# Kernel optimization log

Hardware: AMD Instinct MI355X
Metric: run time of the kernel (lower is better)

Reference implementation:

```python
import jax, jax.numpy as jnp
import numpy as np
import math

CH = 256
NH = 8
HD = CH // NH
GROUPS = 32
EPS = 1e-5


def group_norm(x, gamma, beta):
    # x: [B, C, H, W]; normalize over (C//GROUPS, H, W) per group
    B, C, H, W = x.shape
    xg = x.reshape(B, GROUPS, C // GROUPS, H, W)
    mean = xg.mean(axis=(2, 3, 4), keepdims=True)
    var = xg.var(axis=(2, 3, 4), keepdims=True)
    xg = (xg - mean) * jax.lax.rsqrt(var + EPS)
    x = xg.reshape(B, C, H, W)
    return x * gamma[None, :, None, None] + beta[None, :, None, None]


def setup_inputs() -> dict:
    key = jax.random.key(0)
    ks = jax.random.split(key, 7)
    B, H, W = 2, 64, 64
    x = jax.random.normal(ks[0], (B, CH, H, W), dtype=jnp.float32)
    # conv1x1 weights stored as [out, in] (kernel 1x1 squeezed)
    w_qkv = jax.random.normal(ks[1], (3 * CH, CH), dtype=jnp.float32) * (1.0 / math.sqrt(CH))
    b_qkv = jax.random.normal(ks[2], (3 * CH,), dtype=jnp.float32) * 0.01
    w_proj = jax.random.normal(ks[3], (CH, CH), dtype=jnp.float32) * (1.0 / math.sqrt(CH))
    b_proj = jax.random.normal(ks[4], (CH,), dtype=jnp.float32) * 0.01
    gn_gamma = jnp.ones((CH,), dtype=jnp.float32)
    gn_beta = jnp.zeros((CH,), dtype=jnp.float32)
    return {"x": x, "w_qkv": w_qkv, "b_qkv": b_qkv, "w_proj": w_proj,
            "b_proj": b_proj, "gn_gamma": gn_gamma, "gn_beta": gn_beta}


def reference(x, w_qkv, b_qkv, w_proj, b_proj, gn_gamma, gn_beta):
    B, C, H, W = x.shape
    HW = H * W
    h = group_norm(x, gn_gamma, gn_beta)
    # 1x1 conv == channel matmul
    qkv = jnp.einsum('bchw,oc->bohw', h, w_qkv) + b_qkv[None, :, None, None]
    q, k, v = jnp.split(qkv, 3, axis=1)  # each [B, C, H, W]
    # reshape to heads: q,v -> [B, NH, HW, HD]; k -> [B, NH, HD, HW]
    q = q.reshape(B, NH, HD, HW).transpose(0, 1, 3, 2)
    k = k.reshape(B, NH, HD, HW)
    v = v.reshape(B, NH, HD, HW).transpose(0, 1, 3, 2)
    scale = 1.0 / math.sqrt(HD)
    attn = jnp.einsum('bnqd,bndk->bnqk', q, k) * scale  # [B, NH, HW, HW]
    attn = jax.nn.softmax(attn, axis=-1)
    out = jnp.einsum('bnqk,bnkd->bnqd', attn, v)  # [B, NH, HW, HD]
    out = out.transpose(0, 1, 3, 2).reshape(B, C, H, W)
    out = jnp.einsum('bchw,oc->bohw', out, w_proj) + b_proj[None, :, None, None]
    return x + out
```

## Files before the change

kernel.cpp:

```cpp
#include <hip/hip_runtime.h>
#include <hip/hip_bf16.h>


typedef __attribute__((ext_vector_type(8))) __bf16 bf16x8;
typedef __attribute__((ext_vector_type(4))) float f32x4;
typedef __attribute__((ext_vector_type(2))) float f32x2;
typedef __attribute__((ext_vector_type(16))) float f32x16;
typedef __attribute__((ext_vector_type(2))) unsigned int uint32x2;

#define HW 4096
#define C 256
#define NH 8
#define HD 32
#define QSCALE 0.25505654f
#define KST 36
#define VST 68
#define TST 36
#define NSPLIT 4

__device__ inline unsigned short f2bf(float f) {
  union { float f; unsigned int u; } v; v.f = f;
  unsigned int u = v.u;
  return (unsigned short)((u + 0x7fffu + ((u >> 16) & 1u)) >> 16);
}

__device__ inline bf16x8 load8(const unsigned short* p) {
  bf16x8 v;
  __builtin_memcpy(&v, __builtin_assume_aligned(p, 16), 16);
  return v;
}

__device__ inline bf16x8 load8_lds(const unsigned short* p) {
  uint2 a = *(const uint2*)__builtin_assume_aligned(p, 8);
  uint2 b = *(const uint2*)__builtin_assume_aligned(p + 4, 8);
  union { uint4 u; bf16x8 v; } cv;
  cv.u = make_uint4(a.x, a.y, b.x, b.y);
  return cv.v;
}

__device__ inline unsigned int fbits(float f) {
  unsigned int u; __builtin_memcpy(&u, &f, 4); return u;
}
__device__ inline float bits2f(unsigned int u) {
  float f; __builtin_memcpy(&f, &u, 4); return f;
}

__device__ inline unsigned int pack_bf2(float lo, float hi) {
  return __builtin_amdgcn_perm(fbits(hi) + 0x8000u, fbits(lo) + 0x8000u, 0x07060302u);
}
__device__ inline unsigned int pack_bf2t(float lo, float hi) {
  return __builtin_amdgcn_perm(fbits(hi), fbits(lo), 0x07060302u);
}

__device__ inline size_t toff(int row, int col) {
  return ((size_t)(row >> 6) * 8 + (col >> 5)) * 2048 + (row & 63) * 32 + (col & 31);
}

__global__ __launch_bounds__(256) void gn_stats_part(const float* __restrict__ x,
                                                     float* __restrict__ parts,
                                                     const float* __restrict__ wq,
                                                     const float* __restrict__ wp,
                                                     unsigned short* __restrict__ wq_t,
                                                     unsigned short* __restrict__ wp_t) {
  if (blockIdx.x >= 256) {
    int base = (blockIdx.x - 256) * 1024 + threadIdx.x * 4;
    #pragma unroll
    for (int k = 0; k < 4; k++) {
      int idx = base + k;
      if (idx < 196608) {
        int o = idx >> 8, c = idx & 255;
        wq_t[toff(o, c)] = f2bf(wq[idx]);
      } else {
        int i2 = idx - 196608;
        int o = i2 >> 8, c = i2 & 255;
        wp_t[toff(o, c)] = f2bf(wp[i2]);
      }
    }
    return;
  }
  int i = blockIdx.x;
  const float4* p4 = (const float4*)(x + (size_t)i * 8192);
  int t = threadIdx.x;
  float s = 0.f, ss = 0.f;
  for (int k = t; k < 2048; k += 256) {
    float4 v = p4[k];
    s  += v.x + v.y + v.z + v.w;
    ss += v.x*v.x + v.y*v.y + v.z*v.z + v.w*v.w;
  }
  for (int m = 32; m >= 1; m >>= 1) {
    s  += __shfl_down(s, m, 64);
    ss += __shfl_down(ss, m, 64);
  }
  __shared__ float red[8];
  int w = t >> 6;
  if ((t & 63) == 0) { red[w] = s; red[w + 4] = ss; }
  __syncthreads();
  if (t == 0) {
    parts[i]       = red[0] + red[1] + red[2] + red[3];
    parts[256 + i] = red[4] + red[5] + red[6] + red[7];
  }
}

__global__ __launch_bounds__(256) void gn_apply(const float* __restrict__ x,
                                                const float* __restrict__ parts,
                                                const float* __restrict__ gamma,
                                                const float* __restrict__ beta,
                                                unsigned short* __restrict__ h_t) {
  __shared__ float tile[64][65];
  __shared__ float gmean[8], grstd[8];
  int b = blockIdx.z, c0 = blockIdx.y * 64, s0 = blockIdx.x * 64;
  int t = threadIdx.x;
  if (t < 8) {
    int bg = b * 32 + (c0 >> 3) + t;
    float s  = (parts[4*bg] + parts[4*bg+1]) + (parts[4*bg+2] + parts[4*bg+3]);
    float ss = (parts[256+4*bg] + parts[256+4*bg+1]) + (parts[256+4*bg+2] + parts[256+4*bg+3]);
    float mean = s * (1.0f / 32768.0f);
    float var  = ss * (1.0f / 32768.0f) - mean * mean;
    gmean[t] = mean;
    grstd[t] = rsqrtf(var + 1e-5f);
  }
  const float* xb = x + ((size_t)b * C + c0) * HW + s0;
  #pragma unroll
  for (int k = 0; k < 16; k++) {
    int e = k * 256 + t;
    int i = e >> 6, j = e & 63;
    tile[i][j] = xb[(size_t)i * HW + j];
  }
  __syncthreads();
  unsigned short* hb = h_t + (size_t)b * HW * C +
                       ((size_t)(s0 >> 6) * 8 + (c0 >> 5)) * 2048;
  #pragma unroll
  for (int k = 0; k < 16; k++) {
    int e = k * 256 + t;
    int jr = e >> 6, ir = e & 63;
    int c = c0 + ir, gl = ir >> 3;
    float v = (tile[ir][jr] - gmean[gl]) * grstd[gl] * gamma[c] + beta[c];
    hb[(ir >> 5) * 2048 + jr * 32 + (ir & 31)] = f2bf(v);
  }
}

__global__ __launch_bounds__(256) void qkv_gemm(const unsigned short* __restrict__ wq_t,
                                                const unsigned short* __restrict__ h_t,
                                                const float* __restrict__ b_qkv,
                                                unsigned short* __restrict__ q_t,
                                                unsigned short* __restrict__ k_t,
                                                unsigned short* __restrict__ v_t) {
  int t = threadIdx.x;
  int lane = t & 63, w = t >> 6;
  int quad = lane >> 4, l16 = lane & 15;
  int m0 = blockIdx.y * 64 + w * 16;
  int n0 = blockIdx.x * 64;
  int b  = blockIdx.z;

  __shared__ __align__(16) unsigned short at2[2][64 * TST];
  __shared__ __align__(16) unsigned short bt2[2][64 * TST];

  const uint4* Ag = (const uint4*)(wq_t + (size_t)blockIdx.y * 8 * 2048);
  const uint4* Bg = (const uint4*)(h_t + (size_t)b * HW * C + (size_t)blockIdx.x * 8 * 2048);
  int lrow = t >> 2, lcol = (t & 3) * 8;

  f32x4 acc[4];
  #pragma unroll
  for (int nb = 0; nb < 4; nb++) acc[nb] = (f32x4){0.f, 0.f, 0.f, 0.f};

  uint4 areg = Ag[t];
  uint4 breg = Bg[t];
  int phase = 0;
  for (int k = 0; k < 8; k++, phase ^= 1) {
    unsigned short* ap = &at2[phase][0];
    unsigned short* bp = &bt2[phase][0];
    *(uint2*)(ap + lrow * TST + lcol)     = make_uint2(areg.x, areg.y);
    *(uint2*)(ap + lrow * TST + lcol + 4) = make_uint2(areg.z, areg.w);
    *(uint2*)(bp + lrow * TST + lcol)     = make_uint2(breg.x, breg.y);
    *(uint2*)(bp + lrow * TST + lcol + 4) = make_uint2(breg.z, breg.w);
    int kn = (k < 7) ? k + 1 : 7;
    areg = Ag[kn * 256 + t];
    breg = Bg[kn * 256 + t];
    __syncthreads();
    bf16x8 a = load8_lds(ap + (w * 16 + l16) * TST + quad * 8);
    #pragma unroll
    for (int nb = 0; nb < 4; nb++) {
      bf16x8 bb = load8_lds(bp + (nb * 16 + l16) * TST + quad * 8);
      acc[nb] = __builtin_amdgcn_mfma_f32_16x16x32_bf16(a, bb, acc[nb], 0, 0, 0);
    }
  }

  int seg = m0 >> 8;
  int o0 = m0 + quad * 4;
  #pragma unroll
  for (int nb = 0; nb < 4; nb++) {
    int s = n0 + nb * 16 + l16;
    if (seg == 2) {
      #pragma unroll
      for (int r = 0; r < 4; r++)
        v_t[((size_t)b * C + ((o0 + r) - 512)) * HW + s] = f2bf(acc[nb][r] + b_qkv[o0 + r]);
    } else {
      float sc = seg ? 1.0f : QSCALE;
      float v0 = (acc[nb][0] + b_qkv[o0])     * sc;
      float v1 = (acc[nb][1] + b_qkv[o0 + 1]) * sc;
      float v2 = (acc[nb][2] + b_qkv[o0 + 2]) * sc;
      float v3 = (acc[nb][3] + b_qkv[o0 + 3]) * sc;
      int oc = o0 & 255, h = oc >> 5, d = oc & 31;
      unsigned short* dst = seg ? k_t : q_t;
      uint2 dd;
      dd.x = pack_bf2(v0, v1);
      dd.y = pack_bf2(v2, v3);
      *(uint2*)(dst + (((size_t)b * NH + h) * HW + s) * HD + d) = dd;
    }
  }
}

__device__ __forceinline__ void softmax_frag(const f32x16& S, f32x2& ps2,
                                             bf16x8& f0, bf16x8& f1) {
  float p[16];
  #pragma unroll
  for (int r = 0; r < 16; r++)
    p[r] = __builtin_amdgcn_exp2f(S[r]);
  f32x2 t0 = (f32x2){p[0], p[1]} + (f32x2){p[2], p[3]};
  f32x2 t1 = (f32x2){p[4], p[5]} + (f32x2){p[6], p[7]};
  f32x2 t2 = (f32x2){p[8], p[9]} + (f32x2){p[10], p[11]};
  f32x2 t3 = (f32x2){p[12], p[13]} + (f32x2){p[14], p[15]};
  ps2 += (t0 + t1) + (t2 + t3);
  unsigned int c0 = pack_bf2t(p[0],  p[1]);
  unsigned int c1 = pack_bf2t(p[2],  p[3]);
  unsigned int c2 = pack_bf2t(p[4],  p[5]);
  unsigned int c3 = pack_bf2t(p[6],  p[7]);
  unsigned int c4 = pack_bf2t(p[8],  p[9]);
  unsigned int c5 = pack_bf2t(p[10], p[11]);
  unsigned int c6 = pack_bf2t(p[12], p[13]);
  unsigned int c7 = pack_bf2t(p[14], p[15]);
  uint32x2 s02 = __builtin_amdgcn_permlane32_swap(c0, c2, false, false);
  uint32x2 s13 = __builtin_amdgcn_permlane32_swap(c1, c3, false, false);
  uint32x2 s46 = __builtin_amdgcn_permlane32_swap(c4, c6, false, false);
  uint32x2 s57 = __builtin_amdgcn_permlane32_swap(c5, c7, false, false);
  union { uint4 u; bf16x8 v; } a, b;
  a.u = make_uint4(s02.x, s13.x, s02.y, s13.y);
  b.u = make_uint4(s46.x, s57.x, s46.y, s57.y);
  f0 = a.v;
  f1 = b.v;
}

__global__ __launch_bounds__(256) void flash_part(const unsigned short* __restrict__ q_t,
                                                  const unsigned short* __restrict__ k_t,
                                                  const unsigned short* __restrict__ v_t,
                                                  unsigned short* __restrict__ po,
                                                  float* __restrict__ pl,
                                                  int jspan) {
  int t = threadIdx.x;
  int lane = t & 63, w = t >> 6;
  int n = lane & 31, hi = lane >> 5, hi8 = hi * 8;
  int bh = blockIdx.x, b = bh >> 3, h = bh & 7;
  int m0 = blockIdx.y * 256 + w * 64;
  int z = blockIdx.z;

  __shared__ __align__(16) unsigned short kt2[2][64 * KST];
  __shared__ __align__(16) unsigned short vt2[2][32 * VST];

  const unsigned short* Q  = q_t + (size_t)bh * HW * HD;
  const unsigned short* Kg = k_t + (size_t)bh * HW * HD;
  const unsigned short* Vg = v_t + ((size_t)b * C + h * HD) * HW;

  bf16x8 qa0 = load8(Q + (size_t)(m0 + n) * HD + hi8);
  bf16x8 qa1 = load8(Q + (size_t)(m0 + n) * HD + 16 + hi8);
  bf16x8 qb0 = load8(Q + (size_t)(m0 + 32 + n) * HD + hi8);
  bf16x8 qb1 = load8(Q + (size_t)(m0 + 32 + n) * HD + 16 + hi8);

  int kkey = t >> 2, kseg = (t & 3) * 8;
  int vd   = t >> 3, vseg = (t & 7) * 8;
  const unsigned short* kgp = Kg + (size_t)kkey * HD + kseg;
  const unsigned short* vgp = Vg + (size_t)vd * HW + vseg;

  f32x2 psa = (f32x2){0.f, 0.f};
  f32x2 psb = (f32x2){0.f, 0.f};
  f32x16 oTa = (f32x16){0.f,0.f,0.f,0.f,0.f,0.f,0.f,0.f,0.f,0.f,0.f,0.f,0.f,0.f,0.f,0.f};
  f32x16 oTb = (f32x16){0.f,0.f,0.f,0.f,0.f,0.f,0.f,0.f,0.f,0.f,0.f,0.f,0.f,0.f,0.f,0.f};
  const f32x16 zero16 = (f32x16){0.f,0.f,0.f,0.f,0.f,0.f,0.f,0.f,0.f,0.f,0.f,0.f,0.f,0.f,0.f,0.f};

  int jbase = z * jspan, jend = jbase + jspan;
  uint4 kreg = *(const uint4*)(kgp + (size_t)jbase * HD);
  uint4 vreg = *(const uint4*)(vgp + jbase);

  int phase = 0;
  for (int j0 = jbase; j0 < jend; j0 += 64, phase ^= 1) {
    unsigned short* ktp = &kt2[phase][0];
    unsigned short* vtp = &vt2[phase][0];
    *(uint2*)(ktp + kkey * KST + kseg)     = make_uint2(kreg.x, kreg.y);
    *(uint2*)(ktp + kkey * KST + kseg + 4) = make_uint2(kreg.z, kreg.w);
    *(uint2*)(vtp + vd * VST + vseg)       = make_uint2(vreg.x, vreg.y);
    *(uint2*)(vtp + vd * VST + vseg + 4)   = make_uint2(vreg.z, vreg.w);
    int jn = (j0 + 64 < jend) ? (j0 + 64) : jbase;
    kreg = *(const uint4*)(kgp + (size_t)jn * HD);
    vreg = *(const uint4*)(vgp + jn);
    __syncthreads();

    const unsigned short* kr0 = ktp + n * KST;
    const unsigned short* kr1 = ktp + (32 + n) * KST;
    bf16x8 ka0 = load8_lds(kr0 + hi8);
    bf16x8 ka1 = load8_lds(kr0 + 16 + hi8);
    bf16x8 kb0 = load8_lds(kr1 + hi8);
    bf16x8 kb1 = load8_lds(kr1 + 16 + hi8);

    f32x16 S0 = __builtin_amdgcn_mfma_f32_32x32x16_bf16(ka1, qa1, zero16, 0, 0, 0);
    S0 = __builtin_amdgcn_mfma_f32_32x32x16_bf16(ka0, qa0, S0, 0, 0, 0);
    f32x16 S1 = __builtin_amdgcn_mfma_f32_32x32x16_bf16(kb1, qa1, zero16, 0, 0, 0);
    S1 = __builtin_amdgcn_mfma_f32_32x32x16_bf16(kb0, qa0, S1, 0, 0, 0);
    bf16x8 pf0, pf1, pf2, pf3;
    softmax_frag(S0, psa, pf0, pf1);
    softmax_frag(S1, psa, pf2, pf3);
    const unsigned short* vrow = vtp + n * VST;
    bf16x8 vf0 = load8_lds(vrow + hi8);
    bf16x8 vf1 = load8_lds(vrow + 16 + hi8);
    bf16x8 vf2 = load8_lds(vrow + 32 + hi8);
    bf16x8 vf3 = load8_lds(vrow + 48 + hi8);
    oTa = __builtin_amdgcn_mfma_f32_32x32x16_bf16(vf0, pf0, oTa, 0, 0, 0);
    oTa = __builtin_amdgcn_mfma_f32_32x32x16_bf16(vf1, pf1, oTa, 0, 0, 0);
    oTa = __builtin_amdgcn_mfma_f32_32x32x16_bf16(vf2, pf2, oTa, 0, 0, 0);
    oTa = __builtin_amdgcn_mfma_f32_32x32x16_bf16(vf3, pf3, oTa, 0, 0, 0);

    f32x16 T0 = __builtin_amdgcn_mfma_f32_32x32x16_bf16(ka1, qb1, zero16, 0, 0, 0);
    T0 = __builtin_amdgcn_mfma_f32_32x32x16_bf16(ka0, qb0, T0, 0, 0, 0);
    f32x16 T1 = __builtin_amdgcn_mfma_f32_32x32x16_bf16(kb1, qb1, zero16, 0, 0, 0);
    T1 = __builtin_amdgcn_mfma_f32_32x32x16_bf16(kb0, qb0, T1, 0, 0, 0);
    softmax_frag(T0, psb, pf0, pf1);
    softmax_frag(T1, psb, pf2, pf3);
    oTb = __builtin_amdgcn_mfma_f32_32x32x16_bf16(vf0, pf0, oTb, 0, 0, 0);
    oTb = __builtin_amdgcn_mfma_f32_32x32x16_bf16(vf1, pf1, oTb, 0, 0, 0);
    oTb = __builtin_amdgcn_mfma_f32_32x32x16_bf16(vf2, pf2, oTb, 0, 0, 0);
    oTb = __builtin_amdgcn_mfma_f32_32x32x16_bf16(vf3, pf3, oTb, 0, 0, 0);
  }

  float psuma = psa.x + psa.y;
  psuma += __shfl_xor(psuma, 32, 64);
  float psumb = psb.x + psb.y;
  psumb += __shfl_xor(psumb, 32, 64);

  unsigned short* pra = po + (((size_t)z * 16 + bh) * HW + (m0 + n)) * 32;
  unsigned short* prb = po + (((size_t)z * 16 + bh) * HW + (m0 + 32 + n)) * 32;
  #pragma unroll
  for (int g = 0; g < 4; g++) {
    uint2 dd;
    dd.x = pack_bf2(oTa[4 * g], oTa[4 * g + 1]);
    dd.y = pack_bf2(oTa[4 * g + 2], oTa[4 * g + 3]);
    *(uint2*)(pra + g * 8 + hi * 4) = dd;
    uint2 de;
    de.x = pack_bf2(oTb[4 * g], oTb[4 * g + 1]);
    de.y = pack_bf2(oTb[4 * g + 2], oTb[4 * g + 3]);
    *(uint2*)(prb + g * 8 + hi * 4) = de;
  }
  if (lane < 32) {
    pl[((size_t)z * 16 + bh) * HW + m0 + n] = psuma;
    pl[((size_t)z * 16 + bh) * HW + m0 + 32 + n] = psumb;
  }
}

__global__ __launch_bounds__(256) void merge_parts(const unsigned short* __restrict__ po,
                                                   const float* __restrict__ pl,
                                                   unsigned short* __restrict__ ao_t) {
  int g = blockIdx.x * 256 + threadIdx.x;
  int q4 = g & 3, s = (g >> 2) & 4095, bh = g >> 14;
  const uint4* p4 = (const uint4*)po;
  size_t idx = ((size_t)bh * HW + s) * 4 + q4;
  const size_t zstride = (size_t)16 * HW * 4;
  float acc[8] = {0,0,0,0,0,0,0,0};
  float l = 0.f;
  #pragma unroll
  for (int z = 0; z < NSPLIT; z++) {
    uint4 v = p4[z * zstride + idx];
    acc[0] += bits2f(v.x << 16);  acc[1] += bits2f(v.x & 0xffff0000u);
    acc[2] += bits2f(v.y << 16);  acc[3] += bits2f(v.y & 0xffff0000u);
    acc[4] += bits2f(v.z << 16);  acc[5] += bits2f(v.z & 0xffff0000u);
    acc[6] += bits2f(v.w << 16);  acc[7] += bits2f(v.w & 0xffff0000u);
    l += pl[((size_t)z * 16 + bh) * HW + s];
  }
  float inv = 1.0f / l;
  int b = bh >> 3, h = bh & 7;
  uint4 o;
  o.x = pack_bf2(acc[0] * inv, acc[1] * inv);
  o.y = pack_bf2(acc[2] * inv, acc[3] * inv);
  o.z = pack_bf2(acc[4] * inv, acc[5] * inv);
  o.w = pack_bf2(acc[6] * inv, acc[7] * inv);
  *(uint4*)(ao_t + (size_t)b * HW * C +
            ((size_t)(s >> 6) * 8 + h) * 2048 + (s & 63) * 32 + q4 * 8) = o;
}

__global__ __launch_bounds__(256) void proj_gemm(const unsigned short* __restrict__ wp_t,
                                                 const unsigned short* __restrict__ ao_t,
                                                 const float* __restrict__ b_proj,
                                                 const float* __restrict__ x,
                                                 float* __restrict__ out) {
  int t = threadIdx.x;
  int lane = t & 63, w = t >> 6;
  int quad = lane >> 4, l16 = lane & 15;
  int m0 = blockIdx.y * 64 + w * 16;
  int n0 = blockIdx.x * 64;
  int b  = blockIdx.z;

  __shared__ __align__(16) unsigned short at2[2][64 * TST];
  __shared__ __align__(16) unsigned short bt2[2][64 * TST];

  const uint4* Ag = (const uint4*)(wp_t + (size_t)blockIdx.y * 8 * 2048);
  const uint4* Bg = (const uint4*)(ao_t + (size_t)b * HW * C + (size_t)blockIdx.x * 8 * 2048);
  int lrow = t >> 2, lcol = (t & 3) * 8;

  f32x4 acc[4];
  #pragma unroll
  for (int nb = 0; nb < 4; nb++) acc[nb] = (f32x4){0.f, 0.f, 0.f, 0.f};

  uint4 areg = Ag[t];
  uint4 breg = Bg[t];
  int phase = 0;
  for (int k = 0; k < 8; k++, phase ^= 1) {
    unsigned short* ap = &at2[phase][0];
    unsigned short* bp = &bt2[phase][0];
    *(uint2*)(ap + lrow * TST + lcol)     = make_uint2(areg.x, areg.y);
    *(uint2*)(ap + lrow * TST + lcol + 4) = make_uint2(areg.z, areg.w);
    *(uint2*)(bp + lrow * TST + lcol)     = make_uint2(breg.x, breg.y);
    *(uint2*)(bp + lrow * TST + lcol + 4) = make_uint2(breg.z, breg.w);
    int kn = (k < 7) ? k + 1 : 7;
    areg = Ag[kn * 256 + t];
    breg = Bg[kn * 256 + t];
    __syncthreads();
    bf16x8 a = load8_lds(ap + (w * 16 + l16) * TST + quad * 8);
    #pragma unroll
    for (int nb = 0; nb < 4; nb++) {
      bf16x8 bb = load8_lds(bp + (nb * 16 + l16) * TST + quad * 8);
      acc[nb] = __builtin_amdgcn_mfma_f32_16x16x32_bf16(a, bb, acc[nb], 0, 0, 0);
    }
  }
  #pragma unroll
  for (int nb = 0; nb < 4; nb++) {
    int s = n0 + nb * 16 + l16;
    #pragma unroll
    for (int r = 0; r < 4; r++) {
      int o = m0 + quad * 4 + r;
      size_t idx = ((size_t)b * C + o) * HW + s;
      out[idx] = acc[nb][r] + b_proj[o] + x[idx];
    }
  }
}

extern "C" void kernel_launch(void* const* d_in, const int* in_sizes, int n_in,
                              void* d_out, int out_size, void* d_ws, size_t ws_size,
                              hipStream_t stream) {
  const float* x      = (const float*)d_in[0];
  const float* w_qkv  = (const float*)d_in[1];
  const float* b_qkv  = (const float*)d_in[2];
  const float* w_proj = (const float*)d_in[3];
  const float* b_proj = (const float*)d_in[4];
  const float* gamma  = (const float*)d_in[5];
  const float* beta   = (const float*)d_in[6];
  float* out = (float*)d_out;

  char* ws = (char*)d_ws;
  float*          parts = (float*)ws;
  unsigned short* wq_t  = (unsigned short*)(ws + 4096);
  unsigned short* wp_t  = (unsigned short*)(ws + 397312);
  unsigned short* h_t   = (unsigned short*)(ws + 528384);
  unsigned short* q_t   = (unsigned short*)(ws + 4722688);
  unsigned short* k_t   = (unsigned short*)(ws + 8916992);
  unsigned short* v_t   = (unsigned short*)(ws + 13111296);
  unsigned short* po    = (unsigned short*)(ws + 17305600);
  float*          pl    = (float*)(ws + 34082816);
  unsigned short* ao_t  = h_t;

  gn_stats_part<<<512, 256, 0, stream>>>(x, parts, w_qkv, w_proj, wq_t, wp_t);
  gn_apply<<<dim3(64, 4, 2), 256, 0, stream>>>(x, parts, gamma, beta, h_t);
  qkv_gemm<<<dim3(64, 12, 2), 256, 0, stream>>>(wq_t, h_t, b_qkv, q_t, k_t, v_t);
  flash_part<<<dim3(16, 16, NSPLIT), 256, 0, stream>>>(q_t, k_t, v_t, po, pl, HW / NSPLIT);
  merge_parts<<<1024, 256, 0, stream>>>(po, pl, ao_t);
  proj_gemm<<<dim3(64, 4, 2), 256, 0, stream>>>(wp_t, ao_t, b_proj, x, out);
}
```

Measured before the change: 151.7 us.

## Load K/V fragments directly from global memory, dropping LDS staging and barriers

Removes the double-buffered shared-memory staging of K and V tiles in the flash attention kernel. Each wave now loads its MFMA operand fragments straight from global memory, relying on L1/L2 to share data across the four waves. This eliminates LDS writes, LDS reads and the per-iteration __syncthreads. In exchange it gives up explicit prefetching and multiplies global/cache traffic by four, since each wave fetches the same K/V tile. Load latency is now exposed unless the compiler or other waves hide it.

```diff
diff --git a/kernel.cpp b/kernel.cpp
--- a/kernel.cpp
+++ b/kernel.cpp
@@ -13,8 +13,6 @@
 #define NH 8
 #define HD 32
 #define QSCALE 0.25505654f
-#define KST 36
-#define VST 68
 #define TST 36
 #define NSPLIT 4
 
@@ -253,9 +251,6 @@
   int m0 = blockIdx.y * 256 + w * 64;
   int z = blockIdx.z;
 
-  __shared__ __align__(16) unsigned short kt2[2][64 * KST];
-  __shared__ __align__(16) unsigned short vt2[2][32 * VST];
-
   const unsigned short* Q  = q_t + (size_t)bh * HW * HD;
   const unsigned short* Kg = k_t + (size_t)bh * HW * HD;
   const unsigned short* Vg = v_t + ((size_t)b * C + h * HD) * HW;
@@ -264,11 +259,6 @@
   bf16x8 qa1 = load8(Q + (size_t)(m0 + n) * HD + 16 + hi8);
   bf16x8 qb0 = load8(Q + (size_t)(m0 + 32 + n) * HD + hi8);
   bf16x8 qb1 = load8(Q + (size_t)(m0 + 32 + n) * HD + 16 + hi8);
-
-  int kkey = t >> 2, kseg = (t & 3) * 8;
-  int vd   = t >> 3, vseg = (t & 7) * 8;
-  const unsigned short* kgp = Kg + (size_t)kkey * HD + kseg;
-  const unsigned short* vgp = Vg + (size_t)vd * HW + vseg;
 
   f32x2 psa = (f32x2){0.f, 0.f};
   f32x2 psb = (f32x2){0.f, 0.f};
@@ -277,28 +267,23 @@
   const f32x16 zero16 = (f32x16){0.f,0.f,0.f,0.f,0.f,0.f,0.f,0.f,0.f,0.f,0.f,0.f,0.f,0.f,0.f,0.f};
 
   int jbase = z * jspan, jend = jbase + jspan;
-  uint4 kreg = *(const uint4*)(kgp + (size_t)jbase * HD);
-  uint4 vreg = *(const uint4*)(vgp + jbase);
-
-  int phase = 0;
-  for (int j0 = jbase; j0 < jend; j0 += 64, phase ^= 1) {
-    unsigned short* ktp = &kt2[phase][0];
-    unsigned short* vtp = &vt2[phase][0];
-    *(uint2*)(ktp + kkey * KST + kseg)     = make_uint2(kreg.x, kreg.y);
-    *(uint2*)(ktp + kkey * KST + kseg + 4) = make_uint2(kreg.z, kreg.w);
-    *(uint2*)(vtp + vd * VST + vseg)       = make_uint2(vreg.x, vreg.y);
-    *(uint2*)(vtp + vd * VST + vseg + 4)   = make_uint2(vreg.z, vreg.w);
-    int jn = (j0 + 64 < jend) ? (j0 + 64) : jbase;
-    kreg = *(const uint4*)(kgp + (size_t)jn * HD);
-    vreg = *(const uint4*)(vgp + jn);
-    __syncthreads();
-
-    const unsigned short* kr0 = ktp + n * KST;
-    const unsigned short* kr1 = ktp + (32 + n) * KST;
-    bf16x8 ka0 = load8_lds(kr0 + hi8);
-    bf16x8 ka1 = load8_lds(kr0 + 16 + hi8);
-    bf16x8 kb0 = load8_lds(kr1 + hi8);
-    bf16x8 kb1 = load8_lds(kr1 + 16 + hi8);
+
+  const unsigned short* ka_p = Kg + (size_t)n * HD + hi8;
+  const unsigned short* kb_p = Kg + (size_t)(32 + n) * HD + hi8;
+  const unsigned short* v_p  = Vg + (size_t)n * HW + hi8;
+
+  for (int j0 = jbase; j0 < jend; j0 += 64) {
+    const unsigned short* ka = ka_p + (size_t)j0 * HD;
+    const unsigned short* kb = kb_p + (size_t)j0 * HD;
+    bf16x8 ka0 = load8(ka);
+    bf16x8 ka1 = load8(ka + 16);
+    bf16x8 kb0 = load8(kb);
+    bf16x8 kb1 = load8(kb + 16);
+    const unsigned short* vp = v_p + j0;
+    bf16x8 vf0 = load8(vp);
+    bf16x8 vf1 = load8(vp + 16);
+    bf16x8 vf2 = load8(vp + 32);
+    bf16x8 vf3 = load8(vp + 48);
 
     f32x16 S0 = __builtin_amdgcn_mfma_f32_32x32x16_bf16(ka1, qa1, zero16, 0, 0, 0);
     S0 = __builtin_amdgcn_mfma_f32_32x32x16_bf16(ka0, qa0, S0, 0, 0, 0);
@@ -307,11 +292,6 @@
     bf16x8 pf0, pf1, pf2, pf3;
     softmax_frag(S0, psa, pf0, pf1);
     softmax_frag(S1, psa, pf2, pf3);
-    const unsigned short* vrow = vtp + n * VST;
-    bf16x8 vf0 = load8_lds(vrow + hi8);
-    bf16x8 vf1 = load8_lds(vrow + 16 + hi8);
-    bf16x8 vf2 = load8_lds(vrow + 32 + hi8);
-    bf16x8 vf3 = load8_lds(vrow + 48 + hi8);
     oTa = __builtin_amdgcn_mfma_f32_32x32x16_bf16(vf0, pf0, oTa, 0, 0, 0);
     oTa = __builtin_amdgcn_mfma_f32_32x32x16_bf16(vf1, pf1, oTa, 0, 0, 0);
     oTa = __builtin_amdgcn_mfma_f32_32x32x16_bf16(vf2, pf2, oTa, 0, 0, 0);
```

New measurement: 157.6 us. +3.9%, slower.
